# Performance work log

Hardware: AMD Instinct MI355X
Metric: run time of the kernel (lower is better)

Reference implementation:

```python
import jax, jax.numpy as jnp
import numpy as np

V, E, H, B, T1, T2 = 32000, 300, 300, 64, 48, 48


def _lstm_last(x, Wih, Whh, bih, bhh):
    # x: [T, B, in]; returns final hidden state h_T: [B, H] (PyTorch gate order i,f,g,o)
    h0 = jnp.zeros((x.shape[1], Whh.shape[1]), x.dtype)
    def step(carry, xt):
        h, c = carry
        g = xt @ Wih.T + h @ Whh.T + bih + bhh
        i, f, gc, o = jnp.split(g, 4, axis=-1)
        c = jax.nn.sigmoid(f) * c + jax.nn.sigmoid(i) * jnp.tanh(gc)
        h = jax.nn.sigmoid(o) * jnp.tanh(c)
        return (h, c), None
    (h, _), _ = jax.lax.scan(step, (h0, h0), x)
    return h


def _bilstm_last(x, pf, pr):
    hf = _lstm_last(x, *pf)
    hr = _lstm_last(x[::-1], *pr)
    # faithful quirk: original reverses projr[0] along dim 0 == BATCH dim
    return jnp.concatenate([hf, hr[::-1]], axis=1)  # [B, 2H]


def _forward(x1, x2, x1_mask, x2_mask,
             emb, eW, eU, ebi, ebh, rW, rU, rbi, rbh,
             dW, dU, dbi, dbh, sW, sU, sbi, sbh,
             f1w, f1b, f2w, f2b, fow, fob):
    emb1 = emb[x1]  # [T1,B,E]
    emb2 = emb[x2]
    # encoder outputs final hidden [B,2H], broadcast over time by mask multiply (faithful quirk)
    ctx1 = _bilstm_last(emb1, (eW, eU, ebi, ebh), (rW, rU, rbi, rbh))[None] * x1_mask[:, :, None]  # [T1,B,2H]
    ctx2 = _bilstm_last(emb2, (eW, eU, ebi, ebh), (rW, rU, rbi, rbh))[None] * x2_mask[:, :, None]  # [T2,B,2H]
    c1 = ctx1.transpose(1, 0, 2)  # [B,T1,2H]
    c2 = ctx2.transpose(1, 0, 2)  # [B,T2,2H]
    # scores[b,i,j] = max_d c1[b,i,d]*c2[b,j,d]  (vectorized form of the O(T1*T2) python loop)
    scores = jnp.max(c1[:, :, None, :] * c2[:, None, :, :], axis=-1)  # [B,T1,T2]
    m1 = x1_mask.T  # [B,T1]
    m2 = x2_mask.T  # [B,T2]
    # masked softmax over hypothesis axis (axis=2)
    ea = jnp.exp(scores - jnp.max(scores, axis=2, keepdims=True)) * m2[:, None, :]
    alpha = ea / jnp.sum(ea, axis=2, keepdims=True)  # [B,T1,T2]
    # faithful quirk: MAX (not sum) pooling of attention-weighted hypothesis
    a_tilde = jnp.max(alpha[:, :, :, None] * c2[:, None, :, :], axis=2)  # [B,T1,2H]
    # masked softmax over premise axis (axis=1)
    eb = jnp.exp(scores - jnp.max(scores, axis=1, keepdims=True)) * m1[:, :, None]
    beta = eb / jnp.sum(eb, axis=1, keepdims=True)  # [B,T1,T2]
    b_tilde = jnp.einsum('bij,bid->bjd', beta, c1)  # [B,T2,2H]
    ctx1_ = a_tilde.transpose(1, 0, 2)  # [T1,B,2H]
    ctx2_ = b_tilde.transpose(1, 0, 2)  # [T2,B,2H]
    inp1 = jnp.concatenate([ctx1, ctx1_, ctx1 * ctx1_, ctx1 - ctx1_], axis=2)  # [T1,B,8H]
    inp2 = jnp.concatenate([ctx2, ctx2_, ctx2 * ctx2_, ctx2 - ctx2_], axis=2)
    h1 = jax.nn.relu(inp1 @ f1w.T + f1b)
    h2 = jax.nn.relu(inp2 @ f1w.T + f1b)
    ctx3 = _bilstm_last(h1, (dW, dU, dbi, dbh), (sW, sU, sbi, sbh))  # [B,2H]
    ctx4 = _bilstm_last(h2, (dW, dU, dbi, dbh), (sW, sU, sbi, sbh))  # [B,2H]
    w3 = ctx3[None] * x1_mask[:, :, None]  # [T1,B,2H]
    w4 = ctx4[None] * x2_mask[:, :, None]  # [T2,B,2H]
    logit = jnp.concatenate([
        w3.sum(0) / x1_mask.sum(0)[:, None], w3.max(0),
        w4.sum(0) / x2_mask.sum(0)[:, None], w4.max(0)], axis=1)  # [B,8H]
    logit = jnp.tanh(logit @ f2w.T + f2b)
    return logit @ fow.T + fob  # [B,3]


def setup_inputs() -> dict:
    key = jax.random.key(0)
    ks = jax.random.split(key, 32)
    s = 0.05
    n = lambda k, shape: jax.random.normal(k, shape, jnp.float32) * s
    d = {
        'x1': jax.random.randint(ks[0], (T1, B), 0, V, dtype=jnp.int32),
        'x1_mask': jnp.ones((T1, B), jnp.float32),
        'x2': jax.random.randint(ks[1], (T2, B), 0, V, dtype=jnp.int32),
        'x2_mask': jnp.ones((T2, B), jnp.float32),
        'l': T1,
        'embed_table': n(ks[2], (V, E)),
        'enc_Wih': n(ks[3], (4 * H, E)), 'enc_Whh': n(ks[4], (4 * H, H)),
        'enc_bih': n(ks[5], (4 * H,)), 'enc_bhh': n(ks[6], (4 * H,)),
        'encr_Wih': n(ks[7], (4 * H, E)), 'encr_Whh': n(ks[8], (4 * H, H)),
        'encr_bih': n(ks[9], (4 * H,)), 'encr_bhh': n(ks[10], (4 * H,)),
        'dec_Wih': n(ks[11], (4 * H, H)), 'dec_Whh': n(ks[12], (4 * H, H)),
        'dec_bih': n(ks[13], (4 * H,)), 'dec_bhh': n(ks[14], (4 * H,)),
        'decr_Wih': n(ks[15], (4 * H, H)), 'decr_Whh': n(ks[16], (4 * H, H)),
        'decr_bih': n(ks[17], (4 * H,)), 'decr_bhh': n(ks[18], (4 * H,)),
        'fc1_w': n(ks[19], (H, 8 * H)), 'fc1_b': n(ks[20], (H,)),
        'fc2_w': n(ks[21], (H, 8 * H)), 'fc2_b': n(ks[22], (H,)),
        'fco_w': n(ks[23], (3, H)), 'fco_b': n(ks[24], (3,)),
    }
    return d


def reference(x1, x1_mask, x2, x2_mask, l, embed_table,
              enc_Wih, enc_Whh, enc_bih, enc_bhh,
              encr_Wih, encr_Whh, encr_bih, encr_bhh,
              dec_Wih, dec_Whh, dec_bih, dec_bhh,
              decr_Wih, decr_Whh, decr_bih, decr_bhh,
              fc1_w, fc1_b, fc2_w, fc2_b, fco_w, fco_b):
    del l  # unused in original forward
    return _forward(x1, x2, x1_mask, x2_mask, embed_table,
                    enc_Wih, enc_Whh, enc_bih, enc_bhh,
                    encr_Wih, encr_Whh, encr_bih, encr_bhh,
                    dec_Wih, dec_Whh, dec_bih, dec_bhh,
                    decr_Wih, decr_Whh, decr_bih, decr_bhh,
                    fc1_w, fc1_b, fc2_w, fc2_b, fco_w, fco_b)
```

## Files before the change

kernel.cpp:

```cpp
#include <hip/hip_runtime.h>
#include <math.h>

typedef unsigned short u16;
typedef unsigned int u32;
typedef unsigned long long u64;
typedef __attribute__((ext_vector_type(8))) __bf16 bf16x8;
typedef __attribute__((ext_vector_type(4))) float f32x4;
typedef __attribute__((ext_vector_type(4))) _Float16 f16x4;

#define MR   6144
#define KP1  320
#define NPG  1280
#define NG   1200
#define WSEG 409600
#define UPSEG 409600
#define GT_H 163840

#define OFF_ABF    0UL
#define OFF_WBF    3932160UL
#define OFF_WCF    10485760UL
#define OFF_BIAS   12645760UL
#define OFF_GF     12664960UL
#define OFF_GR     28393600UL
#define OFF_HB     44122240UL
#define OFF_ENC    44286080UL
#define OFF_VB     44593280UL
#define OFF_CO     45822080UL
#define OFF_ATT    46436480UL
#define OFF_PT     46473344UL
#define OFF_LG     47087744UL
#define OFF_UP     47164544UL
#define OFF_HX     50441344UL
#define OFF_BAR    50769024UL

__device__ __forceinline__ float sigf(float x) { return 1.0f / (1.0f + expf(-x)); }
__device__ __forceinline__ float fsig(float x) { return 1.0f / (1.0f + __expf(-x)); }
__device__ __forceinline__ float ftanh(float x) { return 1.0f - 2.0f / (__expf(2.0f * x) + 1.0f); }

__device__ __forceinline__ u16 f2bf(float x) {
    union { float f; u32 u; } v; v.f = x;
    u32 r = v.u + 0x7fffu + ((v.u >> 16) & 1u);
    return (u16)(r >> 16);
}
__device__ __forceinline__ float bf2f(u16 x) {
    union { u32 u; float f; } v; v.u = ((u32)x) << 16; return v.f;
}

__device__ __forceinline__ void gld_lds16(const u16* g, u16* l) {
    __builtin_amdgcn_global_load_lds(
        (const __attribute__((address_space(1))) unsigned int*)g,
        (__attribute__((address_space(3))) unsigned int*)l, 16, 0, 0);
}

__global__ __launch_bounds__(256) void gather_bf(const int* __restrict__ x1,
                                                 const int* __restrict__ x2,
                                                 const float* __restrict__ emb,
                                                 u16* __restrict__ abf) {
    int idx = blockIdx.x * 256 + threadIdx.x;
    if (idx >= MR * KP1) return;
    int r = idx / KP1, k = idx % KP1;
    float v = 0.0f;
    if (k < 300) {
        int t = r >> 7, bc = r & 127;
        int tok = (bc < 64) ? x1[t * 64 + bc] : x2[t * 64 + bc - 64];
        v = emb[tok * 300 + k];
    }
    abf[idx] = f2bf(v);
}

__global__ __launch_bounds__(256) void wconv8_k(const float* __restrict__ w0, const float* __restrict__ w1,
                                                const float* __restrict__ w2, const float* __restrict__ w3,
                                                const float* __restrict__ w4, const float* __restrict__ w5,
                                                const float* __restrict__ w6, const float* __restrict__ w7,
                                                u16* __restrict__ out) {
    int idx = blockIdx.x * 256 + threadIdx.x;
    if (idx >= 8 * NPG * KP1) return;
    int s = idx / (NPG * KP1), rem = idx % (NPG * KP1);
    int r = rem / KP1, k = rem % KP1;
    const float* w = (s == 0) ? w0 : (s == 1) ? w1 : (s == 2) ? w2 : (s == 3) ? w3
                   : (s == 4) ? w4 : (s == 5) ? w5 : (s == 6) ? w6 : w7;
    float v = 0.0f;
    if (r < NG && k < 300) {
        int j = r >> 2, g = r & 3;
        v = w[(g * 300 + j) * 300 + k];
    }
    out[idx] = f2bf(v);
}

__global__ __launch_bounds__(256) void uperm_k(const u16* __restrict__ WU,
                                               u16* __restrict__ UP) {
    int idx = blockIdx.x * 256 + threadIdx.x;
    if (idx >= 4 * UPSEG) return;
    int seg = idx / UPSEG, pos = idx % UPSEG;
    int T = pos / 5120, kt = (pos / 512) % 10, l = (pos >> 3) & 63, e = pos & 7;
    int n = T * 16 + (l & 15);
    int k = kt * 32 + (l >> 4) * 8 + e;
    UP[idx] = WU[(size_t)seg * WSEG + (size_t)n * KP1 + k];
}

__global__ __launch_bounds__(256) void bconv_k(const float* __restrict__ b0i, const float* __restrict__ b0h,
                                               const float* __restrict__ b1i, const float* __restrict__ b1h,
                                               const float* __restrict__ b2i, const float* __restrict__ b2h,
                                               const float* __restrict__ b3i, const float* __restrict__ b3h,
                                               float* __restrict__ out) {
    int idx = blockIdx.x * 256 + threadIdx.x;
    if (idx >= 4 * NG) return;
    int s = idx / NG, n = idx % NG;
    int j = n >> 2, g = n & 3;
    int src = g * 300 + j;
    const float* bi = (s == 0) ? b0i : (s == 1) ? b1i : (s == 2) ? b2i : b3i;
    const float* bh = (s == 0) ? b0h : (s == 1) ? b1h : (s == 2) ? b2h : b3h;
    out[idx] = bi[src] + bh[src];
}

__global__ __launch_bounds__(256) void wcat_k(const float* __restrict__ f1w,
                                              float* __restrict__ wc) {
    int idx = blockIdx.x * 256 + threadIdx.x;
    if (idx >= 300 * 1800) return;
    int n = idx / 1800, k = idx % 1800;
    int nk = n * 2400 + k;
    float v;
    if (k < 600)       v = f1w[nk] + f1w[nk + 1800];
    else if (k < 1200) v = f1w[nk] - f1w[nk + 1200];
    else               v = f1w[nk];
    wc[idx] = v;
}

__global__ __launch_bounds__(256) void gemm_bt(const u16* __restrict__ A,
                                               const u16* __restrict__ B,
                                               const float* __restrict__ bias,
                                               _Float16* __restrict__ Gh) {
    __shared__ __align__(16) u16 smA[128 * 32];
    __shared__ __align__(16) u16 smB[128 * 32];
    int m0 = blockIdx.x * 128, n0 = blockIdx.y * 128;
    int tid = threadIdx.x, ln = tid & 63;
    int wm = (tid >> 6) & 1, wn = tid >> 7;
    int lrow = ln & 15, lq = ln >> 4;
    f32x4 acc[4][4] = {};
    for (int k0 = 0; k0 < KP1; k0 += 32) {
#pragma unroll
        for (int p = 0; p < 2; p++) {
            int e = (p * 256 + tid) * 8;
            int r = e >> 5, kk = e & 31;
            gld_lds16(A + (size_t)(m0 + r) * KP1 + k0 + kk, smA + e);
            gld_lds16(B + (size_t)(n0 + r) * KP1 + k0 + kk, smB + e);
        }
        __syncthreads();
        bf16x8 av[4], bv[4];
#pragma unroll
        for (int i = 0; i < 4; i++) {
            av[i] = *(const bf16x8*)&smA[(wm * 64 + i * 16 + lrow) * 32 + lq * 8];
            bv[i] = *(const bf16x8*)&smB[(wn * 64 + i * 16 + lrow) * 32 + lq * 8];
        }
#pragma unroll
        for (int i = 0; i < 4; i++)
#pragma unroll
            for (int j = 0; j < 4; j++)
                acc[i][j] = __builtin_amdgcn_mfma_f32_16x16x32_bf16(av[i], bv[j], acc[i][j], 0, 0, 0);
        __syncthreads();
    }
    size_t tb = (size_t)blockIdx.x * GT_H + (size_t)blockIdx.y * 16384
              + (size_t)wm * 8192 + (size_t)wn * 2048 + (size_t)ln * 4;
#pragma unroll
    for (int i = 0; i < 4; i++)
#pragma unroll
        for (int j = 0; j < 4; j++) {
            int n = n0 + wn * 64 + j * 16 + lrow;
            f16x4 v;
            if (n < NG) {
                float bb = bias[n];
#pragma unroll
                for (int r = 0; r < 4; r++) v[r] = (_Float16)(acc[i][j][r] + bb);
            } else {
                v = (f16x4)0;
            }
            *(f16x4*)(Gh + tb + (size_t)(i >> 1) * 4096 + (size_t)(((i & 1) * 4 + j)) * 256) = v;
        }
}

__global__ __launch_bounds__(256, 1) void lstm_sync(const _Float16* __restrict__ Gf,
                                                    const _Float16* __restrict__ Gr,
                                                    const u16* __restrict__ Upf,
                                                    const u16* __restrict__ Upr,
                                                    u16* __restrict__ hx,
                                                    u16* __restrict__ hb,
                                                    u32* __restrict__ barbase) {
    int nt = blockIdx.x, dir = blockIdx.y, half = blockIdx.z;
    const _Float16* G = dir ? Gr : Gf;
    const u16* Up = dir ? Upr : Upf;
    u32* bar = barbase + (dir * 2 + half) * 64;

    int tid = threadIdx.x, ln = tid & 63, w = tid >> 6;
    int wm = w & 1, wn = w >> 1;
    int lrow = ln & 15, lq = ln >> 4;

    __shared__ __align__(16) u16 Ulds[80 * 512];
    __shared__ float P[64][132];

    for (int p = 0; p < 20; p++) {
        int e = (p * 256 + tid) * 8;
        gld_lds16(Up + (size_t)nt * 40960 + e, Ulds + e);
    }
    __syncthreads();

    const u64* HXu = (const u64*)hx;
    u32* HXw = (u32*)hx;
    u32* HOw = (u32*)hb;

    int jp = tid & 15, bg = tid >> 4;
    bool jok = !(nt == 9 && jp >= 6);
    float c[4][2];
#pragma unroll
    for (int q = 0; q < 4; q++) { c[q][0] = 0.0f; c[q][1] = 0.0f; }

    const _Float16* Gs = G + (size_t)nt * 16384 + (size_t)half * 8192
                       + (size_t)wm * 4096 + (size_t)wn * 2048 + (size_t)ln * 4;
    f16x4 gpre[8];
    {
        int ttg = dir ? 47 : 0;
        const _Float16* Gt = Gs + (size_t)ttg * GT_H;
#pragma unroll
        for (int f = 0; f < 8; f++) gpre[f] = *(const f16x4*)(Gt + (size_t)f * 256);
    }

    for (int t = 0; t < 48; t++) {
        union { u64 d[2]; bf16x8 v; } hfrag[2][10];
        const u64* hb0 = HXu + ((size_t)(t & 1) * 2 + dir) * 10240;
#pragma unroll
        for (int i = 0; i < 2; i++) {
            int bcg = half * 64 + wm * 32 + i * 16 + lrow;
            const u64* rp = hb0 + (size_t)bcg * 80 + lq * 2;
#pragma unroll
            for (int kt = 0; kt < 10; kt++) {
                hfrag[i][kt].d[0] = __hip_atomic_load(rp + kt * 8,     __ATOMIC_RELAXED, __HIP_MEMORY_SCOPE_AGENT);
                hfrag[i][kt].d[1] = __hip_atomic_load(rp + kt * 8 + 1, __ATOMIC_RELAXED, __HIP_MEMORY_SCOPE_AGENT);
            }
        }

        f32x4 acc[2][4];
#pragma unroll
        for (int i = 0; i < 2; i++)
#pragma unroll
            for (int j = 0; j < 4; j++) {
                f32x4 a;
#pragma unroll
                for (int r = 0; r < 4; r++) a[r] = (float)gpre[i * 4 + j][r];
                acc[i][j] = a;
            }

#pragma unroll
        for (int kt = 0; kt < 10; kt++) {
            bf16x8 bv[4];
#pragma unroll
            for (int j = 0; j < 4; j++)
                bv[j] = *(const bf16x8*)&Ulds[((size_t)(wn * 4 + j) * 10 + kt) * 512 + ln * 8];
#pragma unroll
            for (int i = 0; i < 2; i++)
#pragma unroll
                for (int j = 0; j < 4; j++)
                    acc[i][j] = __builtin_amdgcn_mfma_f32_16x16x32_bf16(hfrag[i][kt].v, bv[j], acc[i][j], 0, 0, 0);
        }

#pragma unroll
        for (int i = 0; i < 2; i++)
#pragma unroll
            for (int j = 0; j < 4; j++) {
                int col = wn * 64 + j * 16 + lrow;
#pragma unroll
                for (int r = 0; r < 4; r++)
                    P[wm * 32 + i * 16 + lq * 4 + r][col] = acc[i][j][r];
            }
        __syncthreads();

        if (t < 47) {
            int ttg = dir ? 46 - t : t + 1;
            const _Float16* Gt = Gs + (size_t)ttg * GT_H;
#pragma unroll
            for (int f = 0; f < 8; f++) gpre[f] = *(const f16x4*)(Gt + (size_t)f * 256);
        }

        if (jok) {
            u32* hxo = HXw + ((size_t)((t + 1) & 1) * 2 + dir) * 20480;
#pragma unroll
            for (int q = 0; q < 4; q++) {
                int bc = bg * 4 + q;
                f32x4 g0 = *(const f32x4*)&P[bc][8 * jp];
                f32x4 g1 = *(const f32x4*)&P[bc][8 * jp + 4];
                float cn0 = fsig(g0[1]) * c[q][0] + fsig(g0[0]) * ftanh(g0[2]);
                float hn0 = fsig(g0[3]) * ftanh(cn0);
                float cn1 = fsig(g1[1]) * c[q][1] + fsig(g1[0]) * ftanh(g1[2]);
                float hn1 = fsig(g1[3]) * ftanh(cn1);
                c[q][0] = cn0; c[q][1] = cn1;
                u32 pk = (u32)f2bf(hn0) | ((u32)f2bf(hn1) << 16);
                int bcg = half * 64 + bc;
                size_t oi = (size_t)bcg * 160 + nt * 16 + jp;
                if (t < 47)
                    __hip_atomic_store(hxo + oi, pk, __ATOMIC_RELAXED, __HIP_MEMORY_SCOPE_AGENT);
                else
                    HOw[(size_t)dir * 20480 + oi] = pk;
            }
        }

        if (t < 47) {
            __syncthreads();
            if (tid == 0) {
                __hip_atomic_fetch_add(bar, 1u, __ATOMIC_RELAXED, __HIP_MEMORY_SCOPE_AGENT);
                u32 tgt = 10u * (u32)(t + 1);
                while (__hip_atomic_load(bar, __ATOMIC_RELAXED, __HIP_MEMORY_SCOPE_AGENT) < tgt)
                    __builtin_amdgcn_s_sleep(2);
            }
            __syncthreads();
        } else {
            __syncthreads();
        }
    }
}

__global__ __launch_bounds__(256) void enc_k(const u16* __restrict__ hF,
                                             const u16* __restrict__ hR,
                                             float* __restrict__ enc) {
    int idx = blockIdx.x * 256 + threadIdx.x;
    if (idx >= 128 * 600) return;
    int bc = idx / 600, d = idx % 600;
    int seq = bc >> 6, b = bc & 63;
    enc[idx] = (d < 300) ? bf2f(hF[bc * KP1 + d])
                         : bf2f(hR[(seq * 64 + 63 - b) * KP1 + d - 300]);
}

__global__ __launch_bounds__(256) void vbuf_k(const float* __restrict__ enc,
                                              float* __restrict__ V) {
    int idx = blockIdx.x * 256 + threadIdx.x;
    if (idx >= 64 * 600) return;
    int b = idx / 600, d = idx % 600;
    float e1 = enc[b * 600 + d], e2 = enc[(64 + b) * 600 + d];
    float p = fmaxf(e2, 0.0f), nn = fminf(e2, 0.0f);
    V[0 * 38400 + idx] = e1;
    V[1 * 38400 + idx] = p;
    V[2 * 38400 + idx] = nn;
    V[3 * 38400 + idx] = e1 * p;
    V[4 * 38400 + idx] = e1 * nn;
    V[5 * 38400 + idx] = e2;
    V[6 * 38400 + idx] = e1;
    V[7 * 38400 + idx] = e1 * e2;
}

__global__ __launch_bounds__(256) void attn_lite(const float* __restrict__ enc,
                                                 const float* __restrict__ x1m,
                                                 const float* __restrict__ x2m,
                                                 float* __restrict__ AMX,
                                                 float* __restrict__ AMN,
                                                 float* __restrict__ SS) {
    int b = blockIdx.x, tid = threadIdx.x;
    __shared__ float sc[48][49];
    __shared__ float rmx[4], rmn[4];
    __shared__ float MxMn[2];
    float mx = -3.4e38f, mn = 3.4e38f;
    for (int d = tid; d < 600; d += 256) {
        float p = enc[b * 600 + d] * enc[(64 + b) * 600 + d];
        mx = fmaxf(mx, p); mn = fminf(mn, p);
    }
    for (int off = 32; off; off >>= 1) {
        mx = fmaxf(mx, __shfl_down(mx, off));
        mn = fminf(mn, __shfl_down(mn, off));
    }
    if ((tid & 63) == 0) { rmx[tid >> 6] = mx; rmn[tid >> 6] = mn; }
    __syncthreads();
    if (tid == 0) {
        MxMn[0] = fmaxf(fmaxf(rmx[0], rmx[1]), fmaxf(rmx[2], rmx[3]));
        MxMn[1] = fminf(fminf(rmn[0], rmn[1]), fminf(rmn[2], rmn[3]));
    }
    __syncthreads();
    float Mx = MxMn[0], Mn = MxMn[1];
    for (int idx = tid; idx < 2304; idx += 256) {
        int i = idx / 48, j = idx % 48;
        float q = x1m[i * 64 + b] * x2m[j * 64 + b];
        sc[i][j] = (q > 0.0f) ? q * Mx : ((q < 0.0f) ? q * Mn : 0.0f);
    }
    __syncthreads();
    if (tid < 48) {
        int i = tid;
        float m = -3.4e38f;
        for (int j = 0; j < 48; j++) m = fmaxf(m, sc[i][j]);
        float sum = 0.0f;
        for (int j = 0; j < 48; j++) sum += expf(sc[i][j] - m) * x2m[j * 64 + b];
        float wmax = -3.4e38f, wmin = 3.4e38f;
        for (int j = 0; j < 48; j++) {
            float w = expf(sc[i][j] - m) * x2m[j * 64 + b] * x2m[j * 64 + b];
            wmax = fmaxf(wmax, w); wmin = fminf(wmin, w);
        }
        AMX[i * 64 + b] = wmax / sum;
        AMN[i * 64 + b] = wmin / sum;
    } else if (tid >= 64 && tid < 112) {
        int j = tid - 64;
        float m = -3.4e38f;
        for (int i = 0; i < 48; i++) m = fmaxf(m, sc[i][j]);
        float sum = 0.0f, sm = 0.0f;
        for (int i = 0; i < 48; i++) {
            float e = expf(sc[i][j] - m) * x1m[i * 64 + b];
            sum += e; sm += e * x1m[i * 64 + b];
        }
        SS[j * 64 + b] = sm / sum;
    }
}

__global__ __launch_bounds__(256) void coeff_gemm(const float* __restrict__ V,
                                                  const float* __restrict__ Wc,
                                                  float* __restrict__ CO) {
    __shared__ float As[16][64];
    __shared__ float Ws[16][64];
    int s = blockIdx.y;
    const int offs[8] = {0, 600, 600, 1200, 1200, 0, 600, 1200};
    int koff = offs[s];
    const float* A = V + (size_t)s * 38400;
    float* C = CO + (size_t)s * 19200;
    int n0 = blockIdx.x * 64;
    int tid = threadIdx.x;
    int lrow = tid >> 2;
    int lk4 = (tid & 3) << 2;
    int tm = (tid & 15) << 2;
    int tn = (tid >> 4) << 2;
    int nW = n0 + lrow;
    float acc[4][4] = {};
    for (int k0 = 0; k0 < 600; k0 += 16) {
        __syncthreads();
#pragma unroll
        for (int q = 0; q < 4; q++) {
            int k = k0 + lk4 + q;
            As[lk4 + q][lrow] = (k < 600) ? A[lrow * 600 + k] : 0.0f;
            Ws[lk4 + q][lrow] = (k < 600 && nW < 300) ? Wc[(size_t)nW * 1800 + koff + k] : 0.0f;
        }
        __syncthreads();
#pragma unroll
        for (int kk = 0; kk < 16; kk++) {
            float a0 = As[kk][tm], a1 = As[kk][tm + 1], a2 = As[kk][tm + 2], a3 = As[kk][tm + 3];
            float w0 = Ws[kk][tn], w1 = Ws[kk][tn + 1], w2 = Ws[kk][tn + 2], w3 = Ws[kk][tn + 3];
            acc[0][0] += a0 * w0; acc[0][1] += a0 * w1; acc[0][2] += a0 * w2; acc[0][3] += a0 * w3;
            acc[1][0] += a1 * w0; acc[1][1] += a1 * w1; acc[1][2] += a1 * w2; acc[1][3] += a1 * w3;
            acc[2][0] += a2 * w0; acc[2][1] += a2 * w1; acc[2][2] += a2 * w2; acc[2][3] += a2 * w3;
            acc[3][0] += a3 * w0; acc[3][1] += a3 * w1; acc[3][2] += a3 * w2; acc[3][3] += a3 * w3;
        }
    }
#pragma unroll
    for (int ii = 0; ii < 4; ii++) {
        int m = tm + ii;
#pragma unroll
        for (int jn = 0; jn < 4; jn++) {
            int n = n0 + tn + jn;
            if (n < 300) C[m * 300 + n] = acc[ii][jn];
        }
    }
}

__global__ __launch_bounds__(320) void combine_k(const float* __restrict__ CO,
                                                 const float* __restrict__ f1b,
                                                 const float* __restrict__ x1m,
                                                 const float* __restrict__ x2m,
                                                 const float* __restrict__ AMX,
                                                 const float* __restrict__ AMN,
                                                 const float* __restrict__ SS,
                                                 u16* __restrict__ OUT) {
    int r = blockIdx.x;
    int t = r >> 7, bc = r & 127;
    int seq = bc >> 6, b = bc & 63;
    int n = threadIdx.x;
    if (n >= 300) return;
    int bn = b * 300 + n;
    float pre;
    if (seq == 0) {
        float m1 = x1m[t * 64 + b], am = AMX[t * 64 + b], an = AMN[t * 64 + b];
        pre = m1 * CO[bn] + am * CO[19200 + bn] + an * CO[2 * 19200 + bn]
            + m1 * am * CO[3 * 19200 + bn] + m1 * an * CO[4 * 19200 + bn] + f1b[n];
    } else {
        float m2 = x2m[t * 64 + b], sv = SS[t * 64 + b];
        pre = m2 * CO[5 * 19200 + bn] + sv * CO[6 * 19200 + bn]
            + m2 * sv * CO[7 * 19200 + bn] + f1b[n];
    }
    OUT[(size_t)r * KP1 + n] = f2bf(fmaxf(pre, 0.0f));
}

__global__ __launch_bounds__(256) void pool_k(const float* __restrict__ dctx,
                                              const float* __restrict__ x1m,
                                              const float* __restrict__ x2m,
                                              float* __restrict__ pooledT) {
    int idx = blockIdx.x * 256 + threadIdx.x;
    if (idx >= 64 * 2400) return;
    int b = idx / 2400, col = idx % 2400;
    int sec = col / 600, d = col % 600;
    const float* msk = (sec < 2) ? x1m : x2m;
    float v = dctx[((sec < 2 ? 0 : 64) + b) * 600 + d];
    float out;
    if ((sec & 1) == 0) {
        float s = 0, sm = 0;
        for (int t = 0; t < 48; t++) { float mv = msk[t * 64 + b]; s += v * mv; sm += mv; }
        out = s / sm;
    } else {
        float m = -3.4e38f;
        for (int t = 0; t < 48; t++) m = fmaxf(m, v * msk[t * 64 + b]);
        out = m;
    }
    pooledT[col * 64 + b] = out;
}

__global__ __launch_bounds__(256) void fc2_k2(const float* __restrict__ pooledT,
                                              const float* __restrict__ f2w,
                                              const float* __restrict__ f2b,
                                              float* __restrict__ logit) {
    __shared__ float wl[2400];
    __shared__ float red[256];
    int n = blockIdx.x;
    for (int i = threadIdx.x; i < 2400; i += 256) wl[i] = f2w[n * 2400 + i];
    __syncthreads();
    int b = threadIdx.x & 63, kc = threadIdx.x >> 6;
    float acc = 0.0f;
    int k0 = kc * 600;
    for (int kk = 0; kk < 600; kk++) acc += pooledT[(k0 + kk) * 64 + b] * wl[k0 + kk];
    red[threadIdx.x] = acc;
    __syncthreads();
    if (threadIdx.x < 64) {
        float s = red[b] + red[64 + b] + red[128 + b] + red[192 + b];
        logit[b * 300 + n] = tanhf(s + f2b[n]);
    }
}

__global__ __launch_bounds__(64) void out_k2(const float* __restrict__ logit,
                                             const float* __restrict__ fow,
                                             const float* __restrict__ fob,
                                             float* __restrict__ out) {
    int b = blockIdx.x, tid = threadIdx.x;
    float p0 = 0, p1 = 0, p2 = 0;
    for (int k = tid; k < 300; k += 64) {
        float l = logit[b * 300 + k];
        p0 += l * fow[k]; p1 += l * fow[300 + k]; p2 += l * fow[600 + k];
    }
    for (int off = 32; off; off >>= 1) {
        p0 += __shfl_down(p0, off);
        p1 += __shfl_down(p1, off);
        p2 += __shfl_down(p2, off);
    }
    if (tid == 0) {
        out[b * 3 + 0] = p0 + fob[0];
        out[b * 3 + 1] = p1 + fob[1];
        out[b * 3 + 2] = p2 + fob[2];
    }
}

extern "C" void kernel_launch(void* const* d_in, const int* in_sizes, int n_in,
                              void* d_out, int out_size, void* d_ws, size_t ws_size,
                              hipStream_t stream) {
    (void)in_sizes; (void)n_in; (void)out_size; (void)ws_size;
    const int*   x1  = (const int*)d_in[0];
    const float* x1m = (const float*)d_in[1];
    const int*   x2  = (const int*)d_in[2];
    const float* x2m = (const float*)d_in[3];
    const float* emb = (const float*)d_in[5];
    const float* eW  = (const float*)d_in[6];
    const float* eU  = (const float*)d_in[7];
    const float* ebi = (const float*)d_in[8];
    const float* ebh = (const float*)d_in[9];
    const float* rW  = (const float*)d_in[10];
    const float* rU  = (const float*)d_in[11];
    const float* rbi = (const float*)d_in[12];
    const float* rbh = (const float*)d_in[13];
    const float* dW  = (const float*)d_in[14];
    const float* dU  = (const float*)d_in[15];
    const float* dbi = (const float*)d_in[16];
    const float* dbh = (const float*)d_in[17];
    const float* sW  = (const float*)d_in[18];
    const float* sU  = (const float*)d_in[19];
    const float* sbi = (const float*)d_in[20];
    const float* sbh = (const float*)d_in[21];
    const float* f1w = (const float*)d_in[22];
    const float* f1b = (const float*)d_in[23];
    const float* f2w = (const float*)d_in[24];
    const float* f2b = (const float*)d_in[25];
    const float* fow = (const float*)d_in[26];
    const float* fob = (const float*)d_in[27];

    char* wsb = (char*)d_ws;
    u16*       ABF  = (u16*)(wsb + OFF_ABF);
    u16*       WBF  = (u16*)(wsb + OFF_WBF);
    float*     WCF  = (float*)(wsb + OFF_WCF);
    float*     BIAS = (float*)(wsb + OFF_BIAS);
    _Float16*  GFh  = (_Float16*)(wsb + OFF_GF);
    _Float16*  GRh  = (_Float16*)(wsb + OFF_GR);
    u16*       HB   = (u16*)(wsb + OFF_HB);
    float*     ENC  = (float*)(wsb + OFF_ENC);
    float*     VB   = (float*)(wsb + OFF_VB);
    float*     CO   = (float*)(wsb + OFF_CO);
    float*     AMX  = (float*)(wsb + OFF_ATT);
    float*     AMN  = AMX + 3072;
    float*     SS   = AMX + 6144;
    float*     PT   = (float*)(wsb + OFF_PT);
    float*     LG   = (float*)(wsb + OFF_LG);
    u16*       UP   = (u16*)(wsb + OFF_UP);
    u16*       HX   = (u16*)(wsb + OFF_HX);
    u32*       BAR  = (u32*)(wsb + OFF_BAR);

    u16* HF0 = HB;
    u16* HR0 = HB + 40960;

    gather_bf<<<dim3((MR * KP1 + 255) / 256), 256, 0, stream>>>(x1, x2, emb, ABF);
    wconv8_k<<<dim3((8 * NPG * KP1 + 255) / 256), 256, 0, stream>>>(eW, rW, dW, sW, eU, rU, dU, sU, WBF);
    uperm_k<<<dim3((4 * UPSEG + 255) / 256), 256, 0, stream>>>(WBF + 4 * WSEG, UP);
    bconv_k<<<dim3((4 * NG + 255) / 256), 256, 0, stream>>>(ebi, ebh, rbi, rbh, dbi, dbh, sbi, sbh, BIAS);
    wcat_k<<<dim3((300 * 1800 + 255) / 256), 256, 0, stream>>>(f1w, WCF);
    hipMemsetAsync(wsb + OFF_BAR, 0, 2048, stream);

    hipMemsetAsync(wsb + OFF_HX, 0, 327680, stream);
    gemm_bt<<<dim3(48, 10), 256, 0, stream>>>(ABF, WBF,        BIAS,      GFh);
    gemm_bt<<<dim3(48, 10), 256, 0, stream>>>(ABF, WBF + WSEG, BIAS + NG, GRh);
    lstm_sync<<<dim3(10, 2, 2), 256, 0, stream>>>(GFh, GRh, UP, UP + UPSEG, HX, HB, BAR);

    enc_k<<<dim3((128 * 600 + 255) / 256), 256, 0, stream>>>(HF0, HR0, ENC);
    vbuf_k<<<dim3((64 * 600 + 255) / 256), 256, 0, stream>>>(ENC, VB);
    attn_lite<<<dim3(64), 256, 0, stream>>>(ENC, x1m, x2m, AMX, AMN, SS);
    coeff_gemm<<<dim3(5, 8), 256, 0, stream>>>(VB, WCF, CO);
    combine_k<<<dim3(6144), 320, 0, stream>>>(CO, f1b, x1m, x2m, AMX, AMN, SS, ABF);

    hipMemsetAsync(wsb + OFF_HX, 0, 327680, stream);
    gemm_bt<<<dim3(48, 10), 256, 0, stream>>>(ABF, WBF + 2 * WSEG, BIAS + 2 * NG, GFh);
    gemm_bt<<<dim3(48, 10), 256, 0, stream>>>(ABF, WBF + 3 * WSEG, BIAS + 3 * NG, GRh);
    lstm_sync<<<dim3(10, 2, 2), 256, 0, stream>>>(GFh, GRh, UP + 2 * UPSEG, UP + 3 * UPSEG, HX, HB, BAR + 1024);

    enc_k<<<dim3((128 * 600 + 255) / 256), 256, 0, stream>>>(HF0, HR0, ENC);
    pool_k<<<dim3((64 * 2400 + 255) / 256), 256, 0, stream>>>(ENC, x1m, x2m, PT);
    fc2_k2<<<dim3(300), 256, 0, stream>>>(PT, f2w, f2b, LG);
    out_k2<<<dim3(64), 64, 0, stream>>>(LG, fow, fob, (float*)d_out);
}
```

Measured before the change: 1.043 ms.

## Replace LSTM grid barrier with step-tagged hidden-state words and LDS staging

The persistent LSTM kernel no longer uses a global atomic counter barrier between timesteps. Each hidden-state word is now written as a 64-bit value carrying the timestep tag, and consumers spin until every word they need carries the expected tag. The hidden state is then staged through a swizzled LDS buffer from which the MFMA A-fragments are read. The exchange buffer reuses the ABF region, which is dead by that point, with a memset before each LSTM launch. This removes the serialized barrier round trip per step, at the cost of doubled exchange traffic, more polling loads, and extra LDS usage.

```diff
diff --git a/kernel.cpp b/kernel.cpp
--- a/kernel.cpp
+++ b/kernel.cpp
@@ -30,8 +30,8 @@
 #define OFF_PT     46473344UL
 #define OFF_LG     47087744UL
 #define OFF_UP     47164544UL
-#define OFF_HX     50441344UL
-#define OFF_BAR    50769024UL
+
+#define HX_BYTES   655360UL
 
 __device__ __forceinline__ float sigf(float x) { return 1.0f / (1.0f + expf(-x)); }
 __device__ __forceinline__ float fsig(float x) { return 1.0f / (1.0f + __expf(-x)); }
@@ -182,19 +182,18 @@
                                                     const _Float16* __restrict__ Gr,
                                                     const u16* __restrict__ Upf,
                                                     const u16* __restrict__ Upr,
-                                                    u16* __restrict__ hx,
-                                                    u16* __restrict__ hb,
-                                                    u32* __restrict__ barbase) {
+                                                    u64* __restrict__ hx,
+                                                    u16* __restrict__ hb) {
     int nt = blockIdx.x, dir = blockIdx.y, half = blockIdx.z;
     const _Float16* G = dir ? Gr : Gf;
     const u16* Up = dir ? Upr : Upf;
-    u32* bar = barbase + (dir * 2 + half) * 64;
 
     int tid = threadIdx.x, ln = tid & 63, w = tid >> 6;
     int wm = w & 1, wn = w >> 1;
     int lrow = ln & 15, lq = ln >> 4;
 
     __shared__ __align__(16) u16 Ulds[80 * 512];
+    __shared__ __align__(16) u32 Hst[64 * 160];
     __shared__ float P[64][132];
 
     for (int p = 0; p < 20; p++) {
@@ -203,12 +202,9 @@
     }
     __syncthreads();
 
-    const u64* HXu = (const u64*)hx;
-    u32* HXw = (u32*)hx;
     u32* HOw = (u32*)hb;
 
     int jp = tid & 15, bg = tid >> 4;
-    bool jok = !(nt == 9 && jp >= 6);
     float c[4][2];
 #pragma unroll
     for (int q = 0; q < 4; q++) { c[q][0] = 0.0f; c[q][1] = 0.0f; }
@@ -224,18 +220,30 @@
     }
 
     for (int t = 0; t < 48; t++) {
-        union { u64 d[2]; bf16x8 v; } hfrag[2][10];
-        const u64* hb0 = HXu + ((size_t)(t & 1) * 2 + dir) * 10240;
-#pragma unroll
-        for (int i = 0; i < 2; i++) {
-            int bcg = half * 64 + wm * 32 + i * 16 + lrow;
-            const u64* rp = hb0 + (size_t)bcg * 80 + lq * 2;
-#pragma unroll
-            for (int kt = 0; kt < 10; kt++) {
-                hfrag[i][kt].d[0] = __hip_atomic_load(rp + kt * 8,     __ATOMIC_RELAXED, __HIP_MEMORY_SCOPE_AGENT);
-                hfrag[i][kt].d[1] = __hip_atomic_load(rp + kt * 8 + 1, __ATOMIC_RELAXED, __HIP_MEMORY_SCOPE_AGENT);
+        {
+            const u64* slab = hx + ((size_t)(t & 1) * 2 + dir) * 20480 + (size_t)half * 10240;
+            u32 want = (u32)t;
+            u32 hv[40];
+            for (;;) {
+                bool ok = true;
+#pragma unroll
+                for (int q = 0; q < 40; q++) {
+                    u64 x = __hip_atomic_load(slab + q * 256 + tid,
+                                              __ATOMIC_RELAXED, __HIP_MEMORY_SCOPE_AGENT);
+                    hv[q] = (u32)x;
+                    ok &= ((u32)(x >> 32) == want);
+                }
+                if (ok) break;
+                __builtin_amdgcn_s_sleep(1);
             }
-        }
+#pragma unroll
+            for (int q = 0; q < 40; q++) {
+                int idx = q * 256 + tid;
+                int row = idx / 160, cc = idx - row * 160;
+                Hst[row * 160 + (cc ^ ((row & 7) << 2))] = hv[q];
+            }
+        }
+        __syncthreads();
 
         f32x4 acc[2][4];
 #pragma unroll
@@ -250,7 +258,13 @@
 
 #pragma unroll
         for (int kt = 0; kt < 10; kt++) {
-            bf16x8 bv[4];
+            bf16x8 av[2], bv[4];
+#pragma unroll
+            for (int i = 0; i < 2; i++) {
+                int row = wm * 32 + i * 16 + lrow;
+                int cc = (kt * 16 + lq * 4) ^ ((row & 7) << 2);
+                av[i] = *(const bf16x8*)&Hst[row * 160 + cc];
+            }
 #pragma unroll
             for (int j = 0; j < 4; j++)
                 bv[j] = *(const bf16x8*)&Ulds[((size_t)(wn * 4 + j) * 10 + kt) * 512 + ln * 8];
@@ -258,7 +272,7 @@
             for (int i = 0; i < 2; i++)
 #pragma unroll
                 for (int j = 0; j < 4; j++)
-                    acc[i][j] = __builtin_amdgcn_mfma_f32_16x16x32_bf16(hfrag[i][kt].v, bv[j], acc[i][j], 0, 0, 0);
+                    acc[i][j] = __builtin_amdgcn_mfma_f32_16x16x32_bf16(av[i], bv[j], acc[i][j], 0, 0, 0);
         }
 
 #pragma unroll
@@ -279,8 +293,9 @@
             for (int f = 0; f < 8; f++) gpre[f] = *(const f16x4*)(Gt + (size_t)f * 256);
         }
 
-        if (jok) {
-            u32* hxo = HXw + ((size_t)((t + 1) & 1) * 2 + dir) * 20480;
+        {
+            u64* hxo = hx + ((size_t)((t + 1) & 1) * 2 + dir) * 20480;
+            u64 tagb = ((u64)(u32)(t + 1)) << 32;
 #pragma unroll
             for (int q = 0; q < 4; q++) {
                 int bc = bg * 4 + q;
@@ -295,24 +310,13 @@
                 int bcg = half * 64 + bc;
                 size_t oi = (size_t)bcg * 160 + nt * 16 + jp;
                 if (t < 47)
-                    __hip_atomic_store(hxo + oi, pk, __ATOMIC_RELAXED, __HIP_MEMORY_SCOPE_AGENT);
+                    __hip_atomic_store(hxo + oi, (u64)pk | tagb,
+                                       __ATOMIC_RELAXED, __HIP_MEMORY_SCOPE_AGENT);
                 else
                     HOw[(size_t)dir * 20480 + oi] = pk;
             }
         }
-
-        if (t < 47) {
-            __syncthreads();
-            if (tid == 0) {
-                __hip_atomic_fetch_add(bar, 1u, __ATOMIC_RELAXED, __HIP_MEMORY_SCOPE_AGENT);
-                u32 tgt = 10u * (u32)(t + 1);
-                while (__hip_atomic_load(bar, __ATOMIC_RELAXED, __HIP_MEMORY_SCOPE_AGENT) < tgt)
-                    __builtin_amdgcn_s_sleep(2);
-            }
-            __syncthreads();
-        } else {
-            __syncthreads();
-        }
+        __syncthreads();
     }
 }
 
@@ -593,8 +597,7 @@
     float*     PT   = (float*)(wsb + OFF_PT);
     float*     LG   = (float*)(wsb + OFF_LG);
     u16*       UP   = (u16*)(wsb + OFF_UP);
-    u16*       HX   = (u16*)(wsb + OFF_HX);
-    u32*       BAR  = (u32*)(wsb + OFF_BAR);
+    u64*       HX64 = (u64*)(wsb + OFF_ABF);
 
     u16* HF0 = HB;
     u16* HR0 = HB + 40960;
@@ -604,12 +607,11 @@
     uperm_k<<<dim3((4 * UPSEG + 255) / 256), 256, 0, stream>>>(WBF + 4 * WSEG, UP);
     bconv_k<<<dim3((4 * NG + 255) / 256), 256, 0, stream>>>(ebi, ebh, rbi, rbh, dbi, dbh, sbi, sbh, BIAS);
     wcat_k<<<dim3((300 * 1800 + 255) / 256), 256, 0, stream>>>(f1w, WCF);
-    hipMemsetAsync(wsb + OFF_BAR, 0, 2048, stream);
-
-    hipMemsetAsync(wsb + OFF_HX, 0, 327680, stream);
+
     gemm_bt<<<dim3(48, 10), 256, 0, stream>>>(ABF, WBF,        BIAS,      GFh);
     gemm_bt<<<dim3(48, 10), 256, 0, stream>>>(ABF, WBF + WSEG, BIAS + NG, GRh);
-    lstm_sync<<<dim3(10, 2, 2), 256, 0, stream>>>(GFh, GRh, UP, UP + UPSEG, HX, HB, BAR);
+    hipMemsetAsync(wsb + OFF_ABF, 0, HX_BYTES, stream);
+    lstm_sync<<<dim3(10, 2, 2), 256, 0, stream>>>(GFh, GRh, UP, UP + UPSEG, HX64, HB);
 
     enc_k<<<dim3((128 * 600 + 255) / 256), 256, 0, stream>>>(HF0, HR0, ENC);
     vbuf_k<<<dim3((64 * 600 + 255) / 256), 256, 0, stream>>>(ENC, VB);
@@ -617,10 +619,10 @@
     coeff_gemm<<<dim3(5, 8), 256, 0, stream>>>(VB, WCF, CO);
     combine_k<<<dim3(6144), 320, 0, stream>>>(CO, f1b, x1m, x2m, AMX, AMN, SS, ABF);
 
-    hipMemsetAsync(wsb + OFF_HX, 0, 327680, stream);
     gemm_bt<<<dim3(48, 10), 256, 0, stream>>>(ABF, WBF + 2 * WSEG, BIAS + 2 * NG, GFh);
     gemm_bt<<<dim3(48, 10), 256, 0, stream>>>(ABF, WBF + 3 * WSEG, BIAS + 3 * NG, GRh);
-    lstm_sync<<<dim3(10, 2, 2), 256, 0, stream>>>(GFh, GRh, UP + 2 * UPSEG, UP + 3 * UPSEG, HX, HB, BAR + 1024);
+    hipMemsetAsync(wsb + OFF_ABF, 0, HX_BYTES, stream);
+    lstm_sync<<<dim3(10, 2, 2), 256, 0, stream>>>(GFh, GRh, UP + 2 * UPSEG, UP + 3 * UPSEG, HX64, HB);
 
     enc_k<<<dim3((128 * 600 + 255) / 256), 256, 0, stream>>>(HF0, HR0, ENC);
     pool_k<<<dim3((64 * 2400 + 255) / 256), 256, 0, stream>>>(ENC, x1m, x2m, PT);
```

Result: faster. 889.7 us (-14.7%).
